# Optimization experiments

Hardware: AMD Instinct MI355X
Metric: run time of the kernel (lower is better)

Reference implementation:

```python
import jax, jax.numpy as jnp
import numpy as np

N_NODES = 10000
N_EDGES = 70000
IN_DIM = 10
HEADS = 6
LIN_OUT = 254
GAT_DIMS = [(256, 508), (512, 250), (256, 120), (128, 20)]  # (in_dim, out_dim) per DeformGAT
NEG_SLOPE = 0.2


def setup_inputs() -> dict:
    key = jax.random.key(0)
    ks = jax.random.split(key, 8)
    inp = {}
    inp["data"] = jax.random.normal(ks[0], (N_NODES, IN_DIM), dtype=jnp.float32)
    inp["edge_idx"] = jax.random.randint(ks[1], (2, N_EDGES), 0, N_NODES)
    inp["bd_mask"] = jax.random.randint(ks[2], (N_NODES,), 0, 2) > 0
    inp["poly_mesh"] = 0
    inp["W_lin"] = jax.random.normal(ks[3], (IN_DIM, LIN_OUT), dtype=jnp.float32) * 0.05
    inp["b_lin"] = jnp.zeros((LIN_OUT,), dtype=jnp.float32)
    for i, (din, dout) in enumerate(GAT_DIMS):
        k1, k2, k3 = jax.random.split(ks[4 + i], 3)
        inp[f"W{i+1}"] = jax.random.normal(k1, (din, HEADS * dout), dtype=jnp.float32) * 0.05
        inp[f"asrc{i+1}"] = jax.random.normal(k2, (HEADS, dout), dtype=jnp.float32) * 0.05
        inp[f"adst{i+1}"] = jax.random.normal(k3, (HEADS, dout), dtype=jnp.float32) * 0.05
    return inp


def deform_gat(coord, feat, src, dst, bd_mask, W, a_src, a_dst, n):
    """One DeformGAT layer: GAT attention over edge list; features aggregated
    (head-averaged, SELU); coords moved to attention-weighted neighbor centroid,
    boundary nodes pinned."""
    H, C = a_src.shape
    x = (feat @ W).reshape(-1, H, C)                       # [N,H,C]
    a_s = jnp.einsum('nhc,hc->nh', x, a_src)               # [N,H]
    a_d = jnp.einsum('nhc,hc->nh', x, a_dst)               # [N,H]
    e = jax.nn.leaky_relu(a_s[src] + a_d[dst], NEG_SLOPE)  # [E,H]
    # segment softmax over incoming edges of each dst node
    m = jax.ops.segment_max(e, dst, num_segments=n)
    m = jnp.where(jnp.isfinite(m), m, 0.0)
    ex = jnp.exp(e - m[dst])
    denom = jax.ops.segment_sum(ex, dst, num_segments=n)
    alpha = ex / jnp.where(denom[dst] > 0, denom[dst], 1.0)        # [E,H]
    agg = jax.ops.segment_sum(alpha[:, :, None] * x[src], dst, num_segments=n)  # [N,H,C]
    out_feat = jax.nn.selu(agg.mean(axis=1))                       # [N,C]
    am = alpha.mean(axis=1)                                        # [E]
    new_coord = jax.ops.segment_sum(am[:, None] * coord[src], dst, num_segments=n)  # [N,2]
    out_coord = jnp.where(bd_mask[:, None], coord, new_coord)
    return out_coord, out_feat


def reference(data, edge_idx, bd_mask, poly_mesh, W_lin, b_lin,
              W1, asrc1, adst1, W2, asrc2, adst2,
              W3, asrc3, adst3, W4, asrc4, adst4):
    n = data.shape[0]
    coords = data[:, 0:2]
    src, dst = edge_idx[0], edge_idx[1]
    h = jax.nn.selu(data @ W_lin + b_lin)                  # [N,254]
    t1 = jnp.concatenate([coords, h], axis=1)              # [N,256]
    c1, f1 = deform_gat(coords, t1, src, dst, bd_mask, W1, asrc1, adst1, n)
    t2 = jnp.concatenate([c1, coords, f1], axis=1)         # [N,512]
    c2, f2 = deform_gat(c1, t2, src, dst, bd_mask, W2, asrc2, adst2, n)
    t3 = jnp.concatenate([c2, c1, coords, f2], axis=1)     # [N,256]
    c3, f3 = deform_gat(c2, t3, src, dst, bd_mask, W3, asrc3, adst3, n)
    t4 = jnp.concatenate([c3, c2, c1, coords, f3], axis=1) # [N,128]
    c4, f4 = deform_gat(c3, t4, src, dst, bd_mask, W4, asrc4, adst4, n)
    return c4
```

## Files before the change

kernel.cpp:

```cpp
#include <hip/hip_runtime.h>
#include <hip/hip_bf16.h>

#define N_NODES 10000
#define N_EDGES 70000
#define HEADS 6
#define MPAD 10112
#define SELU_SCALE 1.0507009873554805f
#define SELU_ALPHA  1.6732632423543772f
#define NEG_SLOPE 0.2f

typedef __attribute__((ext_vector_type(8))) __bf16 bf16x8;
typedef __attribute__((ext_vector_type(4))) float f32x4;

__device__ __forceinline__ float selu_f(float x) {
    return x > 0.f ? SELU_SCALE * x : SELU_SCALE * SELU_ALPHA * (__expf(x) - 1.f);
}
__device__ __forceinline__ unsigned short f2bf(float f) {
    __hip_bfloat16 h = __float2bfloat16(f);
    return __builtin_bit_cast(unsigned short, h);
}
__device__ __forceinline__ float bf2f(unsigned short u) {
    unsigned int x = ((unsigned int)u) << 16;
    return __builtin_bit_cast(float, x);
}

__global__ void count_edges_k(const int* __restrict__ dstv, int* __restrict__ counts) {
    int e = blockIdx.x * blockDim.x + threadIdx.x;
    if (e < N_EDGES) atomicAdd(&counts[dstv[e]], 1);
}

__global__ __launch_bounds__(1024) void scan_k(const int* __restrict__ counts, int* __restrict__ offs) {
    __shared__ int part[1024];
    int tid = threadIdx.x;
    const int per = (N_NODES + 1023) / 1024;
    int start = tid * per;
    int s = 0;
    for (int i = 0; i < per; ++i) { int idx = start + i; if (idx < N_NODES) s += counts[idx]; }
    part[tid] = s;
    __syncthreads();
    for (int off = 1; off < 1024; off <<= 1) {
        int v = (tid >= off) ? part[tid - off] : 0;
        __syncthreads();
        part[tid] += v;
        __syncthreads();
    }
    int run = part[tid] - s;
    for (int i = 0; i < per; ++i) {
        int idx = start + i;
        if (idx < N_NODES) { offs[idx] = run; run += counts[idx]; }
    }
    if (tid == 0) offs[N_NODES] = part[1023];
}

__global__ void fill_csr_k(const int* __restrict__ srcv, const int* __restrict__ dstv,
                           const int* __restrict__ offs,
                           int* __restrict__ cursor, int* __restrict__ srcs) {
    int e = blockIdx.x * blockDim.x + threadIdx.x;
    if (e < N_EDGES) {
        int d = dstv[e];
        int pos = atomicAdd(&cursor[d], 1);
        srcs[offs[d] + pos] = srcv[e];
    }
}

__global__ __launch_bounds__(256) void prep_proj_k(
    const float* __restrict__ data, const float* __restrict__ W, const float* __restrict__ b,
    float* __restrict__ coords0, unsigned short* __restrict__ t1,
    const float* __restrict__ wsf, const float* __restrict__ wdf,
    float* __restrict__ a_s, float* __restrict__ a_d) {
    const int wid = threadIdx.x >> 6, lane = threadIdx.x & 63;
    const int n = blockIdx.x * 4 + wid;
    if (n >= N_NODES) return;
    const int c0 = lane * 4;
    const float* dr = data + (size_t)n * 10;

    float vals[4];
#pragma unroll
    for (int q = 0; q < 4; ++q) {
        int c = c0 + q;
        if (c < 2) {
            vals[q] = dr[c];
        } else {
            int cc = c - 2;
            float acc = b[cc];
#pragma unroll
            for (int k = 0; k < 10; ++k) acc += dr[k] * W[k * 254 + cc];
            vals[q] = selu_f(acc);
        }
    }
    uint2 pk;
    pk.x = (unsigned int)f2bf(vals[0]) | ((unsigned int)f2bf(vals[1]) << 16);
    pk.y = (unsigned int)f2bf(vals[2]) | ((unsigned int)f2bf(vals[3]) << 16);
    *(uint2*)(t1 + (size_t)n * 256 + c0) = pk;
    if (lane == 0) {
        coords0[2 * n] = vals[0];
        coords0[2 * n + 1] = vals[1];
    }

    float s[HEADS] = {}, d[HEADS] = {};
#pragma unroll
    for (int q = 0; q < 4; ++q) {
        float v = bf2f(f2bf(vals[q]));
        const float* ws = wsf + (size_t)(c0 + q) * HEADS;
        const float* wd = wdf + (size_t)(c0 + q) * HEADS;
#pragma unroll
        for (int h = 0; h < HEADS; ++h) {
            s[h] += v * ws[h];
            d[h] += v * wd[h];
        }
    }
#pragma unroll
    for (int off = 32; off > 0; off >>= 1) {
#pragma unroll
        for (int h = 0; h < HEADS; ++h) {
            s[h] += __shfl_xor(s[h], off);
            d[h] += __shfl_xor(d[h], off);
        }
    }
    if (lane == 0) {
#pragma unroll
        for (int h = 0; h < HEADS; ++h) {
            a_s[n * HEADS + h] = s[h];
            a_d[n * HEADS + h] = d[h];
        }
    }
}

__global__ __launch_bounds__(64) void fold_all_k(
    const float* __restrict__ W0, const float* __restrict__ s0v, const float* __restrict__ d0v,
    const float* __restrict__ W1, const float* __restrict__ s1v, const float* __restrict__ d1v,
    const float* __restrict__ W2, const float* __restrict__ s2v, const float* __restrict__ d2v,
    const float* __restrict__ W3, const float* __restrict__ s3v, const float* __restrict__ d3v,
    float* __restrict__ wsf0, float* __restrict__ wdf0,
    float* __restrict__ wsf1, float* __restrict__ wdf1,
    float* __restrict__ wsf2, float* __restrict__ wdf2,
    float* __restrict__ wsf3, float* __restrict__ wdf3) {
    int bid = blockIdx.x;
    const float* W; const float* sv; const float* dv; float* ws; float* wd;
    int K, C, pair;
    if (bid < 1536)      { W = W0; sv = s0v; dv = d0v; ws = wsf0; wd = wdf0; K = 256; C = 508; pair = bid; }
    else if (bid < 4608) { W = W1; sv = s1v; dv = d1v; ws = wsf1; wd = wdf1; K = 512; C = 250; pair = bid - 1536; }
    else if (bid < 6144) { W = W2; sv = s2v; dv = d2v; ws = wsf2; wd = wdf2; K = 256; C = 120; pair = bid - 4608; }
    else                 { W = W3; sv = s3v; dv = d3v; ws = wsf3; wd = wdf3; K = 128; C = 20;  pair = bid - 6144; }
    int k = pair / HEADS, h = pair % HEADS;
    int lane = threadIdx.x;
    const float* wr = W + (size_t)k * (HEADS * C) + h * C;
    const float* sr = sv + h * C;
    const float* dr = dv + h * C;
    float s = 0.f, d = 0.f;
    for (int c = lane; c < C; c += 64) {
        float w = wr[c];
        s += w * sr[c];
        d += w * dr[c];
    }
#pragma unroll
    for (int off = 32; off > 0; off >>= 1) {
        s += __shfl_xor(s, off);
        d += __shfl_xor(d, off);
    }
    if (lane == 0) { ws[pair] = s; wd[pair] = d; }
}

__global__ __launch_bounds__(256) void convv_all_k(
    const float* __restrict__ W0, unsigned short* __restrict__ Vt0,
    const float* __restrict__ W1, unsigned short* __restrict__ Vt1,
    const float* __restrict__ W2, unsigned short* __restrict__ Vt2) {
    __shared__ float tile[64][65];
    int bid = blockIdx.x;
    const float* W; unsigned short* Vt; int K, C, K6, bid2, ktiles;
    if (bid < 192)      { W = W0; Vt = Vt0; K = 256; C = 508; K6 = 1536; bid2 = bid;       ktiles = 24; }
    else if (bid < 384) { W = W1; Vt = Vt1; K = 512; C = 250; K6 = 3072; bid2 = bid - 192; ktiles = 48; }
    else                { W = W2; Vt = Vt2; K = 256; C = 120; K6 = 1536; bid2 = bid - 384; ktiles = 24; }
    int kb = bid2 % ktiles, cb = bid2 / ktiles;
    const int tx = threadIdx.x;
    const int ty = threadIdx.y;
    const int k0 = kb * 64;
    const int c0 = cb * 64;
    for (int i = ty; i < 64; i += 4) {
        int kk = k0 + i;
        int h = kk / K, k = kk - h * K;
        int c = c0 + tx;
        tile[i][tx] = (c < C) ? W[(size_t)k * (HEADS * C) + h * C + c] : 0.f;
    }
    __syncthreads();
    for (int i = ty; i < 64; i += 4) {
        int c = c0 + i;
        Vt[(size_t)c * K6 + k0 + tx] = f2bf(tile[tx][i]);
    }
}

__global__ __launch_bounds__(256) void gemm_split_k(
    const unsigned short* __restrict__ A,
    const unsigned short* __restrict__ Bt,
    unsigned short* __restrict__ part,
    int Kpitch, int klen, int Npad) {
    __shared__ unsigned short lds[16384];
    const int tid = threadIdx.x;
    const int lane = tid & 63, wid = tid >> 6;
    const int wm = wid >> 1, wn = wid & 1;
    const int m0 = blockIdx.y * 128;
    const int n0 = blockIdx.x * 128;
    const int kz = blockIdx.z;
    const int kbeg = kz * klen;

    f32x4 acc[4][4] = {};

    const unsigned short* gsrc[8];
    unsigned ldsoff[8];
#pragma unroll
    for (int i = 0; i < 8; ++i) {
        const int half = i >> 2;
        const int slot = (i & 3) * 256 + tid;
        const int r = slot >> 3;
        const int c16 = slot & 7;
        const int ksl = c16 ^ (r & 7);
        gsrc[i] = (half ? (Bt + (size_t)(n0 + r) * Kpitch) : (A + (size_t)(m0 + r) * Kpitch)) + ksl * 8;
        ldsoff[i] = (unsigned)(half * 8192 + ((i & 3) * 256 + wid * 64) * 8);
    }

    for (int kt = kbeg; kt < kbeg + klen; kt += 64) {
#pragma unroll
        for (int i = 0; i < 8; ++i) {
            __builtin_amdgcn_global_load_lds(
                (const __attribute__((address_space(1))) unsigned int*)(gsrc[i] + kt),
                (__attribute__((address_space(3))) unsigned int*)(&lds[ldsoff[i]]),
                16, 0, 0);
        }
        __syncthreads();
#pragma unroll
        for (int kc = 0; kc < 2; ++kc) {
            const int xo = (((kc * 4 + (lane >> 4)) ^ (lane & 7)) << 4);
            bf16x8 aop[4], bop[4];
#pragma unroll
            for (int f = 0; f < 4; ++f) {
                const int rA = wm * 64 + f * 16 + (lane & 15);
                bop[f] = *(const bf16x8*)((const char*)lds + rA * 128 + xo);
                const int rB = wn * 64 + f * 16 + (lane & 15);
                aop[f] = *(const bf16x8*)((const char*)lds + 16384 * 1 + rB * 128 + xo);
            }
#pragma unroll
            for (int fm = 0; fm < 4; ++fm)
#pragma unroll
                for (int fn = 0; fn < 4; ++fn)
                    acc[fm][fn] = __builtin_amdgcn_mfma_f32_16x16x32_bf16(
                        aop[fn], bop[fm], acc[fm][fn], 0, 0, 0);
        }
        __syncthreads();
    }

    unsigned short* pbase = part + (size_t)kz * MPAD * Npad;
    const int mrow = m0 + wm * 64 + (lane & 15);
    const int ncol = n0 + wn * 64 + ((lane >> 4) * 4);
#pragma unroll
    for (int fm = 0; fm < 4; ++fm) {
#pragma unroll
        for (int fn = 0; fn < 4; ++fn) {
            f32x4 v = acc[fm][fn];
            unsigned int u0 = (unsigned int)f2bf(v.x) | ((unsigned int)f2bf(v.y) << 16);
            unsigned int u1 = (unsigned int)f2bf(v.z) | ((unsigned int)f2bf(v.w) << 16);
            uint2 pk = make_uint2(u0, u1);
            *(uint2*)&pbase[(size_t)(mrow + fm * 16) * Npad + ncol + fn * 16] = pk;
        }
    }
}

template<int KN>
__global__ __launch_bounds__(256) void reduceproj_k(
    const unsigned short* __restrict__ part, int KS, int Npad, int off,
    unsigned short* __restrict__ tnext,
    const float* __restrict__ wsf, const float* __restrict__ wdf,
    float* __restrict__ a_s, float* __restrict__ a_d) {
    const int wid = threadIdx.x >> 6, lane = threadIdx.x & 63;
    const int n = blockIdx.x * 4 + wid;
    if (n >= N_NODES) return;
    constexpr int KPL = KN / 64;
    const int c0 = lane * KPL;
    unsigned short* row = tnext + (size_t)n * KN;

    float vals[KPL];
#pragma unroll
    for (int q = 0; q < KPL; ++q) {
        int c = c0 + q;
        if (c < off) {
            vals[q] = bf2f(row[c]);
        } else {
            int cp = c - off;
            float sum = 0.f;
            for (int kz = 0; kz < KS; ++kz)
                sum += bf2f(part[(size_t)kz * MPAD * Npad + (size_t)n * Npad + cp]);
            float o = selu_f(sum * (1.f / 6.f));
            vals[q] = o;
            row[c] = f2bf(o);
        }
    }

    float s[HEADS] = {}, d[HEADS] = {};
#pragma unroll
    for (int q = 0; q < KPL; ++q) {
        int c = c0 + q;
        float v = vals[q];
        const float* ws = wsf + (size_t)c * HEADS;
        const float* wd = wdf + (size_t)c * HEADS;
#pragma unroll
        for (int h = 0; h < HEADS; ++h) {
            s[h] += v * ws[h];
            d[h] += v * wd[h];
        }
    }
#pragma unroll
    for (int off2 = 32; off2 > 0; off2 >>= 1) {
#pragma unroll
        for (int h = 0; h < HEADS; ++h) {
            s[h] += __shfl_xor(s[h], off2);
            d[h] += __shfl_xor(d[h], off2);
        }
    }
    if (lane == 0) {
#pragma unroll
        for (int h = 0; h < HEADS; ++h) {
            a_s[n * HEADS + h] = s[h];
            a_d[n * HEADS + h] = d[h];
        }
    }
}

template<int KT>
__global__ __launch_bounds__(256) void attn_agg_move_k(
    const float* __restrict__ a_s, const float* __restrict__ a_d,
    const int* __restrict__ srcs, const int* __restrict__ offs,
    const unsigned short* __restrict__ t_in, unsigned short* __restrict__ thagg,
    const float* __restrict__ cprev, const int* __restrict__ bd,
    float* __restrict__ cout, unsigned short* __restrict__ tnext, int ld,
    const float* __restrict__ xA, int offA,
    const float* __restrict__ xB, int offB) {
    const int wid = threadIdx.x >> 6, lane = threadIdx.x & 63;
    const int n = blockIdx.x * 4 + wid;
    if (n >= N_NODES) return;
    const int r0 = offs[n], r1 = offs[n + 1];
    const int deg = r1 - r0;

    float ad[HEADS];
#pragma unroll
    for (int h = 0; h < HEADS; ++h) ad[h] = a_d[n * HEADS + h];

    constexpr int KPL = (KT > 0) ? (KT / 64) : 1;
    float acc[HEADS][KPL] = {};
    float cx = 0.f, cy = 0.f;

    if (deg <= 64) {
        const bool ok = lane < deg;
        const int mysrc = ok ? srcs[r0 + lane] : 0;
        float mm[HEADS], ss[HEADS], myal[HEADS];
#pragma unroll
        for (int h = 0; h < HEADS; ++h) {
            float v = -1e30f;
            if (ok) {
                v = a_s[mysrc * HEADS + h] + ad[h];
                v = v > 0.f ? v : NEG_SLOPE * v;
            }
            mm[h] = v;
        }
#pragma unroll
        for (int off = 32; off > 0; off >>= 1)
#pragma unroll
            for (int h = 0; h < HEADS; ++h) mm[h] = fmaxf(mm[h], __shfl_xor(mm[h], off));
#pragma unroll
        for (int h = 0; h < HEADS; ++h) {
            float v = -1e30f;
            if (ok) {
                v = a_s[mysrc * HEADS + h] + ad[h];
                v = v > 0.f ? v : NEG_SLOPE * v;
            }
            myal[h] = ok ? __expf(v - mm[h]) : 0.f;
            ss[h] = myal[h];
        }
#pragma unroll
        for (int off = 32; off > 0; off >>= 1)
#pragma unroll
            for (int h = 0; h < HEADS; ++h) ss[h] += __shfl_xor(ss[h], off);
        float am = 0.f;
#pragma unroll
        for (int h = 0; h < HEADS; ++h) {
            float rdh = ss[h] > 0.f ? 1.f / ss[h] : 0.f;
            myal[h] *= rdh;
            am += myal[h];
        }
        if (ok) {
            am *= (1.f / 6.f);
            cx = am * cprev[2 * mysrc];
            cy = am * cprev[2 * mysrc + 1];
        }
        if constexpr (KT > 0) {
            for (int j = 0; j < deg; ++j) {
                int src = __shfl(mysrc, j);
                float al[HEADS];
#pragma unroll
                for (int h = 0; h < HEADS; ++h) al[h] = __shfl(myal[h], j);
                if constexpr (KT == 512) {
                    uint4 u = *(const uint4*)(t_in + (size_t)src * 512 + lane * 8);
                    float tv[8];
                    tv[0] = bf2f((unsigned short)(u.x & 0xffff)); tv[1] = bf2f((unsigned short)(u.x >> 16));
                    tv[2] = bf2f((unsigned short)(u.y & 0xffff)); tv[3] = bf2f((unsigned short)(u.y >> 16));
                    tv[4] = bf2f((unsigned short)(u.z & 0xffff)); tv[5] = bf2f((unsigned short)(u.z >> 16));
                    tv[6] = bf2f((unsigned short)(u.w & 0xffff)); tv[7] = bf2f((unsigned short)(u.w >> 16));
#pragma unroll
                    for (int h = 0; h < HEADS; ++h)
#pragma unroll
                        for (int q = 0; q < 8; ++q) acc[h][q] += al[h] * tv[q];
                } else {
                    uint2 u = *(const uint2*)(t_in + (size_t)src * 256 + lane * 4);
                    float tv[4];
                    tv[0] = bf2f((unsigned short)(u.x & 0xffff)); tv[1] = bf2f((unsigned short)(u.x >> 16));
                    tv[2] = bf2f((unsigned short)(u.y & 0xffff)); tv[3] = bf2f((unsigned short)(u.y >> 16));
#pragma unroll
                    for (int h = 0; h < HEADS; ++h)
#pragma unroll
                        for (int q = 0; q < 4; ++q) acc[h][q] += al[h] * tv[q];
                }
            }
        }
    } else {
        float mm[HEADS], ss[HEADS];
#pragma unroll
        for (int h = 0; h < HEADS; ++h) { mm[h] = -1e30f; ss[h] = 0.f; }
        for (int base = r0; base < r1; base += 64) {
            int i = base + lane;
            if (i < r1) {
                int src = srcs[i];
#pragma unroll
                for (int h = 0; h < HEADS; ++h) {
                    float v = a_s[src * HEADS + h] + ad[h];
                    v = v > 0.f ? v : NEG_SLOPE * v;
                    float nm = fmaxf(mm[h], v);
                    ss[h] = ss[h] * __expf(mm[h] - nm) + __expf(v - nm);
                    mm[h] = nm;
                }
            }
        }
#pragma unroll
        for (int off = 32; off > 0; off >>= 1) {
#pragma unroll
            for (int h = 0; h < HEADS; ++h) {
                float mo = __shfl_xor(mm[h], off);
                float so = __shfl_xor(ss[h], off);
                float nm = fmaxf(mm[h], mo);
                ss[h] = ss[h] * __expf(mm[h] - nm) + so * __expf(mo - nm);
                mm[h] = nm;
            }
        }
        float rd[HEADS];
#pragma unroll
        for (int h = 0; h < HEADS; ++h) rd[h] = ss[h] > 0.f ? 1.f / ss[h] : 0.f;

        for (int base = r0; base < r1; base += 64) {
            int i = base + lane;
            bool ok = i < r1;
            int mysrc = ok ? srcs[i] : 0;
            float myal[HEADS];
#pragma unroll
            for (int h = 0; h < HEADS; ++h) myal[h] = 0.f;
            if (ok) {
                float am = 0.f;
#pragma unroll
                for (int h = 0; h < HEADS; ++h) {
                    float v = a_s[mysrc * HEADS + h] + ad[h];
                    v = v > 0.f ? v : NEG_SLOPE * v;
                    float a = __expf(v - mm[h]) * rd[h];
                    myal[h] = a;
                    am += a;
                }
                am *= (1.f / 6.f);
                cx += am * cprev[2 * mysrc];
                cy += am * cprev[2 * mysrc + 1];
            }
            if constexpr (KT > 0) {
                int cnt = min(64, r1 - base);
                for (int j = 0; j < cnt; ++j) {
                    int src = __shfl(mysrc, j);
                    float al[HEADS];
#pragma unroll
                    for (int h = 0; h < HEADS; ++h) al[h] = __shfl(myal[h], j);
                    if constexpr (KT == 512) {
                        uint4 u = *(const uint4*)(t_in + (size_t)src * 512 + lane * 8);
                        float tv[8];
                        tv[0] = bf2f((unsigned short)(u.x & 0xffff)); tv[1] = bf2f((unsigned short)(u.x >> 16));
                        tv[2] = bf2f((unsigned short)(u.y & 0xffff)); tv[3] = bf2f((unsigned short)(u.y >> 16));
                        tv[4] = bf2f((unsigned short)(u.z & 0xffff)); tv[5] = bf2f((unsigned short)(u.z >> 16));
                        tv[6] = bf2f((unsigned short)(u.w & 0xffff)); tv[7] = bf2f((unsigned short)(u.w >> 16));
#pragma unroll
                        for (int h = 0; h < HEADS; ++h)
#pragma unroll
                            for (int q = 0; q < 8; ++q) acc[h][q] += al[h] * tv[q];
                    } else {
                        uint2 u = *(const uint2*)(t_in + (size_t)src * 256 + lane * 4);
                        float tv[4];
                        tv[0] = bf2f((unsigned short)(u.x & 0xffff)); tv[1] = bf2f((unsigned short)(u.x >> 16));
                        tv[2] = bf2f((unsigned short)(u.y & 0xffff)); tv[3] = bf2f((unsigned short)(u.y >> 16));
#pragma unroll
                        for (int h = 0; h < HEADS; ++h)
#pragma unroll
                            for (int q = 0; q < 4; ++q) acc[h][q] += al[h] * tv[q];
                    }
                }
            }
        }
    }

    if constexpr (KT == 512) {
#pragma unroll
        for (int h = 0; h < HEADS; ++h) {
            uint4 pk;
            pk.x = (unsigned int)f2bf(acc[h][0]) | ((unsigned int)f2bf(acc[h][1]) << 16);
            pk.y = (unsigned int)f2bf(acc[h][2]) | ((unsigned int)f2bf(acc[h][3]) << 16);
            pk.z = (unsigned int)f2bf(acc[h][4]) | ((unsigned int)f2bf(acc[h][5]) << 16);
            pk.w = (unsigned int)f2bf(acc[h][6]) | ((unsigned int)f2bf(acc[h][7]) << 16);
            *(uint4*)(thagg + (size_t)n * 3072 + h * 512 + lane * 8) = pk;
        }
    } else if constexpr (KT == 256) {
#pragma unroll
        for (int h = 0; h < HEADS; ++h) {
            uint2 pk;
            pk.x = (unsigned int)f2bf(acc[h][0]) | ((unsigned int)f2bf(acc[h][1]) << 16);
            pk.y = (unsigned int)f2bf(acc[h][2]) | ((unsigned int)f2bf(acc[h][3]) << 16);
            *(uint2*)(thagg + (size_t)n * 1536 + h * 256 + lane * 4) = pk;
        }
    }
#pragma unroll
    for (int off = 32; off > 0; off >>= 1) {
        cx += __shfl_xor(cx, off);
        cy += __shfl_xor(cy, off);
    }
    if (lane == 0) {
        float px = cprev[2 * n], py = cprev[2 * n + 1];
        float ocx, ocy;
        if (bd[n] != 0) { ocx = px; ocy = py; }
        else { ocx = cx; ocy = cy; }
        cout[2 * n] = ocx; cout[2 * n + 1] = ocy;
        if (tnext) {
            unsigned short* row = tnext + (size_t)n * ld;
            row[0] = f2bf(ocx); row[1] = f2bf(ocy);
            row[2] = f2bf(px);  row[3] = f2bf(py);
            if (xA) { row[offA] = f2bf(xA[2 * n]); row[offA + 1] = f2bf(xA[2 * n + 1]); }
            if (xB) { row[offB] = f2bf(xB[2 * n]); row[offB + 1] = f2bf(xB[2 * n + 1]); }
        }
    }
}

static inline int cdiv(int a, int b) { return (a + b - 1) / b; }

extern "C" void kernel_launch(void* const* d_in, const int* in_sizes, int n_in,
                              void* d_out, int out_size, void* d_ws, size_t ws_size,
                              hipStream_t stream) {
    const float* data = (const float*)d_in[0];
    const int* eidx = (const int*)d_in[1];
    const int* bd = (const int*)d_in[2];
    const float* W_lin = (const float*)d_in[4];
    const float* b_lin = (const float*)d_in[5];
    const float* Wl[4]  = {(const float*)d_in[6],  (const float*)d_in[9],
                           (const float*)d_in[12], (const float*)d_in[15]};
    const float* Asrc[4] = {(const float*)d_in[7],  (const float*)d_in[10],
                            (const float*)d_in[13], (const float*)d_in[16]};
    const float* Adst[4] = {(const float*)d_in[8],  (const float*)d_in[11],
                            (const float*)d_in[14], (const float*)d_in[17]};
    const int Kd[4] = {256, 512, 256, 128};
    const int Cpadd[4] = {512, 256, 128, 0};
    const int KSd[4] = {2, 4, 4, 0};

    const int* srcv = eidx;
    const int* dstv = eidx + N_EDGES;

    char* p = (char*)d_ws;
    auto alloc = [&](size_t bytes) -> void* {
        void* r = (void*)p;
        p += (bytes + 255) & ~(size_t)255;
        return r;
    };
    unsigned short* tb1 = (unsigned short*)alloc((size_t)MPAD * 256 * 2);
    unsigned short* tb2 = (unsigned short*)alloc((size_t)MPAD * 512 * 2);
    unsigned short* tb3 = (unsigned short*)alloc((size_t)MPAD * 256 * 2);
    unsigned short* tb4 = (unsigned short*)alloc((size_t)MPAD * 128 * 2);
    unsigned short* thagg = (unsigned short*)alloc((size_t)MPAD * 3072 * 2);
    unsigned short* VtL[3];
    VtL[0] = (unsigned short*)alloc((size_t)512 * 1536 * 2);
    VtL[1] = (unsigned short*)alloc((size_t)256 * 3072 * 2);
    VtL[2] = (unsigned short*)alloc((size_t)128 * 1536 * 2);
    unsigned short* partb = (unsigned short*)alloc((size_t)8 * MPAD * 256 * 2);
    float* coords0 = (float*)alloc((size_t)N_NODES * 2 * 4);
    float* c1 = (float*)alloc((size_t)N_NODES * 2 * 4);
    float* c2 = (float*)alloc((size_t)N_NODES * 2 * 4);
    float* c3 = (float*)alloc((size_t)N_NODES * 2 * 4);
    float* a_s = (float*)alloc((size_t)N_NODES * HEADS * 4);
    float* a_d = (float*)alloc((size_t)N_NODES * HEADS * 4);
    float* wsfL[4]; float* wdfL[4];
    wsfL[0] = (float*)alloc(1536 * 4); wdfL[0] = (float*)alloc(1536 * 4);
    wsfL[1] = (float*)alloc(3072 * 4); wdfL[1] = (float*)alloc(3072 * 4);
    wsfL[2] = (float*)alloc(1536 * 4); wdfL[2] = (float*)alloc(1536 * 4);
    wsfL[3] = (float*)alloc(768 * 4);  wdfL[3] = (float*)alloc(768 * 4);
    int* counts = (int*)alloc((size_t)N_NODES * 4);
    int* cursor = (int*)alloc((size_t)N_NODES * 4);
    int* offs = (int*)alloc((size_t)(N_NODES + 1) * 4);
    int* srcs = (int*)alloc((size_t)N_EDGES * 4);

    hipMemsetAsync(counts, 0, (size_t)((char*)offs - (char*)counts), stream);
    count_edges_k<<<cdiv(N_EDGES, 256), 256, 0, stream>>>(dstv, counts);
    scan_k<<<1, 1024, 0, stream>>>(counts, offs);
    fill_csr_k<<<cdiv(N_EDGES, 256), 256, 0, stream>>>(srcv, dstv, offs, cursor, srcs);

    fold_all_k<<<6912, 64, 0, stream>>>(
        Wl[0], Asrc[0], Adst[0], Wl[1], Asrc[1], Adst[1],
        Wl[2], Asrc[2], Adst[2], Wl[3], Asrc[3], Adst[3],
        wsfL[0], wdfL[0], wsfL[1], wdfL[1], wsfL[2], wdfL[2], wsfL[3], wdfL[3]);
    convv_all_k<<<432, dim3(64, 4), 0, stream>>>(Wl[0], VtL[0], Wl[1], VtL[1], Wl[2], VtL[2]);
    prep_proj_k<<<cdiv(N_NODES, 4), 256, 0, stream>>>(
        data, W_lin, b_lin, coords0, tb1, wsfL[0], wdfL[0], a_s, a_d);

    unsigned short* tin[4]   = {tb1, tb2, tb3, tb4};
    unsigned short* tnext[4] = {tb2, tb3, tb4, nullptr};
    int ldn[4]  = {512, 256, 128, 0};
    int foff[4] = {4, 6, 8, 0};
    float* cprev[4] = {coords0, c1, c2, c3};
    float* cout[4]  = {c1, c2, c3, (float*)d_out};
    const float* xAv[4] = {nullptr, coords0, c1, nullptr};
    int offAv[4] = {0, 4, 4, 0};
    const float* xBv[4] = {nullptr, nullptr, coords0, nullptr};
    int offBv[4] = {0, 0, 6, 0};

    for (int l = 0; l < 4; ++l) {
        int K = Kd[l], Cpad = Cpadd[l], KS = KSd[l];
        int K6 = K * HEADS;

        if (l == 3) {
            attn_agg_move_k<0><<<cdiv(N_NODES, 4), 256, 0, stream>>>(
                a_s, a_d, srcs, offs, tin[l], nullptr,
                cprev[l], bd, cout[l], tnext[l], ldn[l],
                xAv[l], offAv[l], xBv[l], offBv[l]);
        } else if (K == 512) {
            attn_agg_move_k<512><<<cdiv(N_NODES, 4), 256, 0, stream>>>(
                a_s, a_d, srcs, offs, tin[l], thagg,
                cprev[l], bd, cout[l], tnext[l], ldn[l],
                xAv[l], offAv[l], xBv[l], offBv[l]);
        } else {
            attn_agg_move_k<256><<<cdiv(N_NODES, 4), 256, 0, stream>>>(
                a_s, a_d, srcs, offs, tin[l], thagg,
                cprev[l], bd, cout[l], tnext[l], ldn[l],
                xAv[l], offAv[l], xBv[l], offBv[l]);
        }

        if (l < 3) {
            int klen = K6 / KS;
            gemm_split_k<<<dim3(Cpad / 128, MPAD / 128, KS), 256, 0, stream>>>(
                thagg, VtL[l], partb, K6, klen, Cpad);
            if (ldn[l] == 512) {
                reduceproj_k<512><<<cdiv(N_NODES, 4), 256, 0, stream>>>(
                    partb, KS, Cpad, foff[l], tnext[l], wsfL[l + 1], wdfL[l + 1], a_s, a_d);
            } else if (ldn[l] == 256) {
                reduceproj_k<256><<<cdiv(N_NODES, 4), 256, 0, stream>>>(
                    partb, KS, Cpad, foff[l], tnext[l], wsfL[l + 1], wdfL[l + 1], a_s, a_d);
            } else {
                reduceproj_k<128><<<cdiv(N_NODES, 4), 256, 0, stream>>>(
                    partb, KS, Cpad, foff[l], tnext[l], wsfL[l + 1], wdfL[l + 1], a_s, a_d);
            }
        }
    }
}
```

Before: 341.3 us.

## Double-buffer LDS in split-K GEMM and vectorize reduceproj bf16 accesses

The split-K GEMM now uses two LDS buffers and issues the async global-to-LDS loads for the next K tile before computing the current one. A manual vmcnt wait replaces the full syncthreads so memory latency can overlap with MFMA work. The reduceproj kernel reads and writes bf16 values in pairs through 32-bit accesses, halving its memory instruction count. Doubling LDS to 64KB per block may reduce occupancy.

```diff
diff --git a/kernel.cpp b/kernel.cpp
--- a/kernel.cpp
+++ b/kernel.cpp
@@ -194,7 +194,7 @@
     const unsigned short* __restrict__ Bt,
     unsigned short* __restrict__ part,
     int Kpitch, int klen, int Npad) {
-    __shared__ unsigned short lds[16384];
+    __shared__ unsigned short lds[2][16384];
     const int tid = threadIdx.x;
     const int lane = tid & 63, wid = tid >> 6;
     const int wm = wid >> 1, wn = wid & 1;
@@ -202,6 +202,7 @@
     const int n0 = blockIdx.x * 128;
     const int kz = blockIdx.z;
     const int kbeg = kz * klen;
+    const int nt = klen >> 6;
 
     f32x4 acc[4][4] = {};
 
@@ -218,15 +219,28 @@
         ldsoff[i] = (unsigned)(half * 8192 + ((i & 3) * 256 + wid * 64) * 8);
     }
 
-    for (int kt = kbeg; kt < kbeg + klen; kt += 64) {
+    auto stage = [&](int kt, int buf) {
 #pragma unroll
         for (int i = 0; i < 8; ++i) {
             __builtin_amdgcn_global_load_lds(
                 (const __attribute__((address_space(1))) unsigned int*)(gsrc[i] + kt),
-                (__attribute__((address_space(3))) unsigned int*)(&lds[ldsoff[i]]),
+                (__attribute__((address_space(3))) unsigned int*)(&lds[buf][ldsoff[i]]),
                 16, 0, 0);
         }
-        __syncthreads();
+    };
+
+    stage(kbeg, 0);
+    for (int t = 0; t < nt; ++t) {
+        const int cur = t & 1;
+        if (t + 1 < nt) {
+            stage(kbeg + (t + 1) * 64, cur ^ 1);
+            asm volatile("s_waitcnt vmcnt(8)" ::: "memory");
+        } else {
+            asm volatile("s_waitcnt vmcnt(0)" ::: "memory");
+        }
+        __builtin_amdgcn_sched_barrier(0);
+        __builtin_amdgcn_s_barrier();
+        const char* base = (const char*)(&lds[cur][0]);
 #pragma unroll
         for (int kc = 0; kc < 2; ++kc) {
             const int xo = (((kc * 4 + (lane >> 4)) ^ (lane & 7)) << 4);
@@ -234,9 +248,9 @@
 #pragma unroll
             for (int f = 0; f < 4; ++f) {
                 const int rA = wm * 64 + f * 16 + (lane & 15);
-                bop[f] = *(const bf16x8*)((const char*)lds + rA * 128 + xo);
+                bop[f] = *(const bf16x8*)(base + rA * 128 + xo);
                 const int rB = wn * 64 + f * 16 + (lane & 15);
-                aop[f] = *(const bf16x8*)((const char*)lds + 16384 * 1 + rB * 128 + xo);
+                aop[f] = *(const bf16x8*)(base + 16384 + rB * 128 + xo);
             }
 #pragma unroll
             for (int fm = 0; fm < 4; ++fm)
@@ -245,7 +259,7 @@
                     acc[fm][fn] = __builtin_amdgcn_mfma_f32_16x16x32_bf16(
                         aop[fn], bop[fm], acc[fm][fn], 0, 0, 0);
         }
-        __syncthreads();
+        __builtin_amdgcn_s_barrier();
     }
 
     unsigned short* pbase = part + (size_t)kz * MPAD * Npad;
@@ -279,18 +293,26 @@
 
     float vals[KPL];
 #pragma unroll
-    for (int q = 0; q < KPL; ++q) {
+    for (int q = 0; q < KPL; q += 2) {
         int c = c0 + q;
         if (c < off) {
-            vals[q] = bf2f(row[c]);
+            unsigned int u = *(const unsigned int*)(row + c);
+            vals[q] = bf2f((unsigned short)(u & 0xffff));
+            vals[q + 1] = bf2f((unsigned short)(u >> 16));
         } else {
             int cp = c - off;
-            float sum = 0.f;
-            for (int kz = 0; kz < KS; ++kz)
-                sum += bf2f(part[(size_t)kz * MPAD * Npad + (size_t)n * Npad + cp]);
-            float o = selu_f(sum * (1.f / 6.f));
-            vals[q] = o;
-            row[c] = f2bf(o);
+            float s0 = 0.f, s1 = 0.f;
+            for (int kz = 0; kz < KS; ++kz) {
+                unsigned int u = *(const unsigned int*)(part + (size_t)kz * MPAD * Npad
+                                                       + (size_t)n * Npad + cp);
+                s0 += bf2f((unsigned short)(u & 0xffff));
+                s1 += bf2f((unsigned short)(u >> 16));
+            }
+            float o0 = selu_f(s0 * (1.f / 6.f));
+            float o1 = selu_f(s1 * (1.f / 6.f));
+            vals[q] = o0; vals[q + 1] = o1;
+            *(unsigned int*)(row + c) =
+                (unsigned int)f2bf(o0) | ((unsigned int)f2bf(o1) << 16);
         }
     }
 
```

New measurement: 309.8 us. 1.1x faster.
